# Performance work log

Measured on AMD Instinct MI355X. Metric: run time of the kernel, lower is better.

The kernel has to match this reference:

```python
import jax, jax.numpy as jnp
import numpy as np

N_NODES = 100000
DIM = 64
N_EDGES = 1250000
PRESERVE = 0.1  # preserve_ratio in GCN module


def gcn_conv(x, W, b, row, col, edge_w, num_nodes):
    """PyG GCNConv with normalize=True: symmetric norm with added self-loops.
    x: [N, d], W: [d, d_out], edge (row -> col) with weight edge_w: [E].
    """
    # add self-loops with weight 1
    loop = jnp.arange(num_nodes, dtype=row.dtype)
    r = jnp.concatenate([row, loop])
    c = jnp.concatenate([col, loop])
    w = jnp.concatenate([edge_w, jnp.ones((num_nodes,), dtype=edge_w.dtype)])
    # symmetric degree normalization: deg computed at target (col)
    deg = jax.ops.segment_sum(w, c, num_segments=num_nodes)
    dinv = jnp.where(deg > 0, jax.lax.rsqrt(deg), 0.0)
    norm = dinv[r] * w * dinv[c]  # [E+N]
    xw = x @ W  # [N, d_out] (linear transform before propagation)
    msg = xw[r] * norm[:, None]  # gather + scale
    out = jax.ops.segment_sum(msg, c, num_segments=num_nodes)  # scatter-add at targets
    return out + b


def setup_inputs() -> dict:
    key = jax.random.key(0)
    ks = jax.random.split(key, 8)
    skill_embed = jax.random.normal(ks[0], (N_NODES, DIM), dtype=jnp.float32)
    edge_index = jax.random.randint(ks[1], (2, N_EDGES), 0, N_NODES, dtype=jnp.int64)
    edge_attr = jax.random.uniform(ks[2], (N_EDGES,), dtype=jnp.float32)
    # GCNConv params (W stored as [in, out] here), glorot-ish init
    scale = 1.0 / np.sqrt(DIM)
    W1 = jax.random.uniform(ks[3], (DIM, DIM), minval=-scale, maxval=scale, dtype=jnp.float32)
    b1 = jnp.zeros((DIM,), dtype=jnp.float32)
    W2 = jax.random.uniform(ks[4], (DIM, DIM), minval=-scale, maxval=scale, dtype=jnp.float32)
    b2 = jnp.zeros((DIM,), dtype=jnp.float32)
    return {"skill_embed": skill_embed, "edge_index": edge_index, "edge_attr": edge_attr,
            "W1": W1, "b1": b1, "W2": W2, "b2": b2}


def reference(skill_embed, edge_index, edge_attr, W1, b1, W2, b2):
    row, col = edge_index[0], edge_index[1]
    n = skill_embed.shape[0]
    temp = skill_embed
    out = gcn_conv(skill_embed, W1, b1, row, col, edge_attr, n)
    temp = (1.0 - PRESERVE) * out + PRESERVE * temp
    out = gcn_conv(temp, W2, b2, row, col, edge_attr, n)
    temp = (1.0 - PRESERVE) * out + PRESERVE * temp
    return temp
```

## Files before the change

kernel.cpp:

```cpp
#include <hip/hip_runtime.h>

#define DIM 64
#define PRESERVE 0.1f

typedef unsigned short bf16_t;

__device__ __forceinline__ float readlane_f(float v, int l) {
    return __int_as_float(__builtin_amdgcn_readlane(__float_as_int(v), l));
}
__device__ __forceinline__ float bf2f(bf16_t u) {
    return __uint_as_float(((unsigned)u) << 16);
}
__device__ __forceinline__ bf16_t f2bf(float f) {
    unsigned u = __float_as_uint(f);
    unsigned r = (u + 0x7FFFu + ((u >> 16) & 1u)) >> 16;
    return (bf16_t)r;
}

__global__ void k_init(int* cursor, int n) {
    int i = blockIdx.x * blockDim.x + threadIdx.x;
    if (i < n) cursor[i] = 0;
}

__global__ void k_hist4(const int4* __restrict__ col4, int* cursor,
                        int4* __restrict__ rank4, int nthreads) {
    int t = blockIdx.x * blockDim.x + threadIdx.x;
    if (t >= nthreads) return;
    int4 c = col4[t];
    int4 r;
    r.x = atomicAdd(&cursor[c.x], 1);
    r.y = atomicAdd(&cursor[c.y], 1);
    r.z = atomicAdd(&cursor[c.z], 1);
    r.w = atomicAdd(&cursor[c.w], 1);
    rank4[t] = r;
}

__global__ void k_hist1(const int* __restrict__ col, int* cursor,
                        int* __restrict__ rank, int E) {
    int e = blockIdx.x * blockDim.x + threadIdx.x;
    if (e < E) rank[e] = atomicAdd(&cursor[col[e]], 1);
}

__global__ __launch_bounds__(256) void k_scan1(const int* __restrict__ counts,
                                               int* __restrict__ offsets,
                                               int* __restrict__ blksum, int n) {
    __shared__ int s[256];
    int t = threadIdx.x;
    int idx = blockIdx.x * 256 + t;
    int v = (idx < n) ? counts[idx] : 0;
    s[t] = v;
    __syncthreads();
    for (int off = 1; off < 256; off <<= 1) {
        int x = (t >= off) ? s[t - off] : 0;
        __syncthreads();
        s[t] += x;
        __syncthreads();
    }
    if (idx < n) offsets[idx] = s[t];
    if (t == 255) blksum[blockIdx.x] = s[255];
}

__global__ __launch_bounds__(512) void k_scan2(const int* __restrict__ blksum,
                                               int* __restrict__ blkoff, int nblk) {
    __shared__ int s[512];
    int t = threadIdx.x;
    int v = (t < nblk) ? blksum[t] : 0;
    s[t] = v;
    __syncthreads();
    for (int off = 1; off < 512; off <<= 1) {
        int x = (t >= off) ? s[t - off] : 0;
        __syncthreads();
        s[t] += x;
        __syncthreads();
    }
    if (t < nblk) blkoff[t] = s[t] - v;
}

__global__ __launch_bounds__(256) void k_scan3(const int* __restrict__ counts,
                                               int* __restrict__ offsets,
                                               const int* __restrict__ blkoff,
                                               int n, int E) {
    int t = threadIdx.x;
    int idx = blockIdx.x * 256 + t;
    if (idx < n) offsets[idx] = offsets[idx] - counts[idx] + blkoff[blockIdx.x];
    if (idx == 0) offsets[n] = E;
}

__global__ void k_fill4(const int4* __restrict__ row4, const int4* __restrict__ col4,
                        const float4* __restrict__ w4, const int4* __restrict__ rank4,
                        const int* __restrict__ offsets, int2* __restrict__ sedge,
                        int nthreads) {
    int t = blockIdx.x * blockDim.x + threadIdx.x;
    if (t >= nthreads) return;
    int4 r = row4[t];
    int4 c = col4[t];
    float4 w = w4[t];
    int4 k = rank4[t];
    int2 p;
    p.x = r.x; p.y = __float_as_int(w.x); sedge[offsets[c.x] + k.x] = p;
    p.x = r.y; p.y = __float_as_int(w.y); sedge[offsets[c.y] + k.y] = p;
    p.x = r.z; p.y = __float_as_int(w.z); sedge[offsets[c.z] + k.z] = p;
    p.x = r.w; p.y = __float_as_int(w.w); sedge[offsets[c.w] + k.w] = p;
}

__global__ void k_fill1(const int* __restrict__ row, const int* __restrict__ col,
                        const float* __restrict__ w, const int* __restrict__ rank,
                        const int* __restrict__ offsets, int2* __restrict__ sedge,
                        int E) {
    int e = blockIdx.x * blockDim.x + threadIdx.x;
    if (e >= E) return;
    int2 p;
    p.x = row[e];
    p.y = __float_as_int(w[e]);
    sedge[offsets[col[e]] + rank[e]] = p;
}

__global__ __launch_bounds__(256) void k_deg_seg(const int2* __restrict__ sedge,
                                                 const int* __restrict__ offsets,
                                                 float* __restrict__ dinv, int n) {
    int tid = threadIdx.x;
    int lane = tid & 63;
    int c = blockIdx.x * 4 + (tid >> 6);
    if (c >= n) return;
    int beg = offsets[c];
    int end = offsets[c + 1];
    float s = 0.0f;
    for (int j = beg + lane; j < end; j += 64) s += __int_as_float(sedge[j].y);
    for (int off = 32; off > 0; off >>= 1) s += __shfl_xor(s, off);
    if (lane == 0) {
        float d = 1.0f + s;
        dinv[c] = (d > 0.0f) ? rsqrtf(d) : 0.0f;
    }
}

__global__ __launch_bounds__(256) void k_mm(
        const float* __restrict__ x, const float* __restrict__ W,
        const float* __restrict__ dinv, bf16_t* __restrict__ xs, int n) {
    int tid = threadIdx.x;
    int lane = tid & 63;
    int waveId = blockIdx.x * 4 + (tid >> 6);
    int nWaves = gridDim.x * 4;

    float Wr[DIM];
#pragma unroll
    for (int k = 0; k < DIM; ++k) Wr[k] = W[k * DIM + lane];

    for (int r0 = waveId * 4; r0 < n; r0 += nWaves * 4) {
        if (r0 + 3 < n) {
            float x0 = x[(size_t)(r0 + 0) * DIM + lane];
            float x1 = x[(size_t)(r0 + 1) * DIM + lane];
            float x2 = x[(size_t)(r0 + 2) * DIM + lane];
            float x3 = x[(size_t)(r0 + 3) * DIM + lane];
            float a0 = 0.f, a1 = 0.f, a2 = 0.f, a3 = 0.f;
#pragma unroll
            for (int k = 0; k < DIM; ++k) {
                float w = Wr[k];
                a0 += readlane_f(x0, k) * w;
                a1 += readlane_f(x1, k) * w;
                a2 += readlane_f(x2, k) * w;
                a3 += readlane_f(x3, k) * w;
            }
            xs[(size_t)(r0 + 0) * DIM + lane] = f2bf(a0 * dinv[r0 + 0]);
            xs[(size_t)(r0 + 1) * DIM + lane] = f2bf(a1 * dinv[r0 + 1]);
            xs[(size_t)(r0 + 2) * DIM + lane] = f2bf(a2 * dinv[r0 + 2]);
            xs[(size_t)(r0 + 3) * DIM + lane] = f2bf(a3 * dinv[r0 + 3]);
        } else {
            for (int r = r0; r < n; ++r) {
                float xv = x[(size_t)r * DIM + lane];
                float a = 0.f;
#pragma unroll
                for (int k = 0; k < DIM; ++k) a += readlane_f(xv, k) * Wr[k];
                xs[(size_t)r * DIM + lane] = f2bf(a * dinv[r]);
            }
        }
    }
}

__global__ __launch_bounds__(256) void k_gather(
        const bf16_t* __restrict__ xs, const int* __restrict__ offsets,
        const int2* __restrict__ sedge, const float* __restrict__ dinv,
        const float* __restrict__ b, const float* __restrict__ xprev,
        float* __restrict__ out, int n) {
    int tid = threadIdx.x;
    int lane = tid & 63;
    int c = blockIdx.x * 4 + (tid >> 6);
    if (c >= n) return;
    float di = dinv[c];
    float acc = bf2f(xs[(size_t)c * DIM + lane]);
    int beg = offsets[c];
    int end = offsets[c + 1];
    for (int b0 = beg; b0 < end; b0 += 64) {
        int m = end - b0;
        if (m > 64) m = 64;
        int r_l = 0, w_l = 0;
        if (lane < m) {
            int2 p = sedge[b0 + lane];
            r_l = p.x;
            w_l = p.y;
        }
        int j = 0;
        for (; j + 3 < m; j += 4) {
            int r0 = __builtin_amdgcn_readlane(r_l, j);
            int r1 = __builtin_amdgcn_readlane(r_l, j + 1);
            int r2 = __builtin_amdgcn_readlane(r_l, j + 2);
            int r3 = __builtin_amdgcn_readlane(r_l, j + 3);
            float w0 = readlane_f(__int_as_float(w_l), j);
            float w1 = readlane_f(__int_as_float(w_l), j + 1);
            float w2 = readlane_f(__int_as_float(w_l), j + 2);
            float w3 = readlane_f(__int_as_float(w_l), j + 3);
            float a0 = bf2f(xs[(size_t)r0 * DIM + lane]);
            float a1 = bf2f(xs[(size_t)r1 * DIM + lane]);
            float a2 = bf2f(xs[(size_t)r2 * DIM + lane]);
            float a3 = bf2f(xs[(size_t)r3 * DIM + lane]);
            acc += a0 * w0;
            acc += a1 * w1;
            acc += a2 * w2;
            acc += a3 * w3;
        }
        for (; j < m; ++j) {
            int r0 = __builtin_amdgcn_readlane(r_l, j);
            float w0 = readlane_f(__int_as_float(w_l), j);
            acc += bf2f(xs[(size_t)r0 * DIM + lane]) * w0;
        }
    }
    float v = (1.0f - PRESERVE) * (acc * di + b[lane]) + PRESERVE * xprev[(size_t)c * DIM + lane];
    out[(size_t)c * DIM + lane] = v;
}

extern "C" void kernel_launch(void* const* d_in, const int* in_sizes, int n_in,
                              void* d_out, int out_size, void* d_ws, size_t ws_size,
                              hipStream_t stream) {
    const float* x  = (const float*)d_in[0];
    const int*   ei = (const int*)d_in[1];
    const float* ew = (const float*)d_in[2];
    const float* W1 = (const float*)d_in[3];
    const float* b1 = (const float*)d_in[4];
    const float* W2 = (const float*)d_in[5];
    const float* b2 = (const float*)d_in[6];

    const int N = in_sizes[0] / DIM;
    const int E = in_sizes[2];
    const int* row = ei;
    const int* col = ei + E;

    int2* sedge   = (int2*)d_ws;
    float* dinv   = (float*)(sedge + E);
    float* temp   = dinv + N;
    bf16_t* xs    = (bf16_t*)(temp + (size_t)N * DIM);
    int* rank     = (int*)(xs + (size_t)N * DIM);
    int* cursor   = rank + E;
    int* offsets  = cursor + N;
    int* blksum   = offsets + N + 1;
    int* blkoff   = blksum + 640;

    const int B = 256;
    const int nblkN = (N + B - 1) / B;
    const int nblkG = (N + 3) / 4;
    const int nblkMM = 1024;

    k_init<<<nblkN, B, 0, stream>>>(cursor, N);

    if ((E & 3) == 0) {
        int nt = E / 4;
        k_hist4<<<(nt + B - 1) / B, B, 0, stream>>>((const int4*)col, cursor, (int4*)rank, nt);
    } else {
        k_hist1<<<(E + B - 1) / B, B, 0, stream>>>(col, cursor, rank, E);
    }

    k_scan1<<<nblkN, B, 0, stream>>>(cursor, offsets, blksum, N);
    k_scan2<<<1, 512, 0, stream>>>(blksum, blkoff, nblkN);
    k_scan3<<<nblkN, B, 0, stream>>>(cursor, offsets, blkoff, N, E);

    if ((E & 3) == 0) {
        int nt = E / 4;
        k_fill4<<<(nt + B - 1) / B, B, 0, stream>>>((const int4*)row, (const int4*)col,
                                                    (const float4*)ew, (const int4*)rank,
                                                    offsets, sedge, nt);
    } else {
        k_fill1<<<(E + B - 1) / B, B, 0, stream>>>(row, col, ew, rank, offsets, sedge, E);
    }

    k_deg_seg<<<nblkG, B, 0, stream>>>(sedge, offsets, dinv, N);

    k_mm<<<nblkMM, B, 0, stream>>>(x, W1, dinv, xs, N);
    k_gather<<<nblkG, B, 0, stream>>>(xs, offsets, sedge, dinv, b1, x, temp, N);

    k_mm<<<nblkMM, B, 0, stream>>>(temp, W2, dinv, xs, N);
    k_gather<<<nblkG, B, 0, stream>>>(xs, offsets, sedge, dinv, b2, temp, (float*)d_out, N);
}
```

Measured before the change: 332.9 us.

## Replace per-edge rank array with 8 privatized counter copies for CSR build

The histogram now spreads its atomics over 8 privatized counter arrays chosen by block index, which is meant to cut contention. It no longer stores a per-edge rank. The scan sums the copies and turns each copy into a starting cursor, and the fill pass claims slots with a second round of atomics instead of reading the stored ranks. This drops the rank array traffic but adds atomics to the fill kernel, and the init and scan passes touch 8x more counter memory. Edge order within a segment becomes nondeterministic.

```diff
diff --git a/kernel.cpp b/kernel.cpp
--- a/kernel.cpp
+++ b/kernel.cpp
@@ -2,6 +2,7 @@
 
 #define DIM 64
 #define PRESERVE 0.1f
+#define NCOPY 8
 
 typedef unsigned short bf16_t;
 
@@ -17,37 +18,42 @@
     return (bf16_t)r;
 }
 
-__global__ void k_init(int* cursor, int n) {
+__global__ void k_init(int* cnt8, int n) {
     int i = blockIdx.x * blockDim.x + threadIdx.x;
-    if (i < n) cursor[i] = 0;
-}
-
-__global__ void k_hist4(const int4* __restrict__ col4, int* cursor,
-                        int4* __restrict__ rank4, int nthreads) {
+    if (i < n) cnt8[i] = 0;
+}
+
+__global__ void k_hist4(const int4* __restrict__ col4, int* __restrict__ cnt8,
+                        int nthreads, int N) {
     int t = blockIdx.x * blockDim.x + threadIdx.x;
     if (t >= nthreads) return;
+    int* cur = cnt8 + (size_t)(blockIdx.x & (NCOPY - 1)) * N;
     int4 c = col4[t];
-    int4 r;
-    r.x = atomicAdd(&cursor[c.x], 1);
-    r.y = atomicAdd(&cursor[c.y], 1);
-    r.z = atomicAdd(&cursor[c.z], 1);
-    r.w = atomicAdd(&cursor[c.w], 1);
-    rank4[t] = r;
-}
-
-__global__ void k_hist1(const int* __restrict__ col, int* cursor,
-                        int* __restrict__ rank, int E) {
+    atomicAdd(&cur[c.x], 1);
+    atomicAdd(&cur[c.y], 1);
+    atomicAdd(&cur[c.z], 1);
+    atomicAdd(&cur[c.w], 1);
+}
+
+__global__ void k_hist1(const int* __restrict__ col, int* __restrict__ cnt8,
+                        int E, int N) {
     int e = blockIdx.x * blockDim.x + threadIdx.x;
-    if (e < E) rank[e] = atomicAdd(&cursor[col[e]], 1);
-}
-
-__global__ __launch_bounds__(256) void k_scan1(const int* __restrict__ counts,
+    if (e >= E) return;
+    int* cur = cnt8 + (size_t)(blockIdx.x & (NCOPY - 1)) * N;
+    atomicAdd(&cur[col[e]], 1);
+}
+
+__global__ __launch_bounds__(256) void k_scan1(const int* __restrict__ cnt8,
                                                int* __restrict__ offsets,
                                                int* __restrict__ blksum, int n) {
     __shared__ int s[256];
     int t = threadIdx.x;
     int idx = blockIdx.x * 256 + t;
-    int v = (idx < n) ? counts[idx] : 0;
+    int v = 0;
+    if (idx < n) {
+#pragma unroll
+        for (int x = 0; x < NCOPY; ++x) v += cnt8[(size_t)x * n + idx];
+    }
     s[t] = v;
     __syncthreads();
     for (int off = 1; off < 256; off <<= 1) {
@@ -76,43 +82,57 @@
     if (t < nblk) blkoff[t] = s[t] - v;
 }
 
-__global__ __launch_bounds__(256) void k_scan3(const int* __restrict__ counts,
+__global__ __launch_bounds__(256) void k_scan3(int* __restrict__ cnt8,
                                                int* __restrict__ offsets,
                                                const int* __restrict__ blkoff,
                                                int n, int E) {
-    int t = threadIdx.x;
-    int idx = blockIdx.x * 256 + t;
-    if (idx < n) offsets[idx] = offsets[idx] - counts[idx] + blkoff[blockIdx.x];
+    int idx = blockIdx.x * 256 + threadIdx.x;
     if (idx == 0) offsets[n] = E;
+    if (idx >= n) return;
+    int c[NCOPY];
+    int tot = 0;
+#pragma unroll
+    for (int x = 0; x < NCOPY; ++x) {
+        c[x] = cnt8[(size_t)x * n + idx];
+        tot += c[x];
+    }
+    int off = offsets[idx] - tot + blkoff[blockIdx.x];
+    offsets[idx] = off;
+#pragma unroll
+    for (int x = 0; x < NCOPY; ++x) {
+        cnt8[(size_t)x * n + idx] = off;
+        off += c[x];
+    }
 }
 
 __global__ void k_fill4(const int4* __restrict__ row4, const int4* __restrict__ col4,
-                        const float4* __restrict__ w4, const int4* __restrict__ rank4,
-                        const int* __restrict__ offsets, int2* __restrict__ sedge,
-                        int nthreads) {
+                        const float4* __restrict__ w4, int* __restrict__ cnt8,
+                        int2* __restrict__ sedge, int nthreads, int N) {
     int t = blockIdx.x * blockDim.x + threadIdx.x;
     if (t >= nthreads) return;
+    int* cur = cnt8 + (size_t)(blockIdx.x & (NCOPY - 1)) * N;
     int4 r = row4[t];
     int4 c = col4[t];
     float4 w = w4[t];
-    int4 k = rank4[t];
     int2 p;
-    p.x = r.x; p.y = __float_as_int(w.x); sedge[offsets[c.x] + k.x] = p;
-    p.x = r.y; p.y = __float_as_int(w.y); sedge[offsets[c.y] + k.y] = p;
-    p.x = r.z; p.y = __float_as_int(w.z); sedge[offsets[c.z] + k.z] = p;
-    p.x = r.w; p.y = __float_as_int(w.w); sedge[offsets[c.w] + k.w] = p;
+    int pos;
+    pos = atomicAdd(&cur[c.x], 1); p.x = r.x; p.y = __float_as_int(w.x); sedge[pos] = p;
+    pos = atomicAdd(&cur[c.y], 1); p.x = r.y; p.y = __float_as_int(w.y); sedge[pos] = p;
+    pos = atomicAdd(&cur[c.z], 1); p.x = r.z; p.y = __float_as_int(w.z); sedge[pos] = p;
+    pos = atomicAdd(&cur[c.w], 1); p.x = r.w; p.y = __float_as_int(w.w); sedge[pos] = p;
 }
 
 __global__ void k_fill1(const int* __restrict__ row, const int* __restrict__ col,
-                        const float* __restrict__ w, const int* __restrict__ rank,
-                        const int* __restrict__ offsets, int2* __restrict__ sedge,
-                        int E) {
+                        const float* __restrict__ w, int* __restrict__ cnt8,
+                        int2* __restrict__ sedge, int E, int N) {
     int e = blockIdx.x * blockDim.x + threadIdx.x;
     if (e >= E) return;
+    int* cur = cnt8 + (size_t)(blockIdx.x & (NCOPY - 1)) * N;
+    int pos = atomicAdd(&cur[col[e]], 1);
     int2 p;
     p.x = row[e];
     p.y = __float_as_int(w[e]);
-    sedge[offsets[col[e]] + rank[e]] = p;
+    sedge[pos] = p;
 }
 
 __global__ __launch_bounds__(256) void k_deg_seg(const int2* __restrict__ sedge,
@@ -247,9 +267,8 @@
     float* dinv   = (float*)(sedge + E);
     float* temp   = dinv + N;
     bf16_t* xs    = (bf16_t*)(temp + (size_t)N * DIM);
-    int* rank     = (int*)(xs + (size_t)N * DIM);
-    int* cursor   = rank + E;
-    int* offsets  = cursor + N;
+    int* cnt8     = (int*)(xs + (size_t)N * DIM);
+    int* offsets  = cnt8 + (size_t)NCOPY * N;
     int* blksum   = offsets + N + 1;
     int* blkoff   = blksum + 640;
 
@@ -258,26 +277,25 @@
     const int nblkG = (N + 3) / 4;
     const int nblkMM = 1024;
 
-    k_init<<<nblkN, B, 0, stream>>>(cursor, N);
+    k_init<<<(NCOPY * N + B - 1) / B, B, 0, stream>>>(cnt8, NCOPY * N);
 
     if ((E & 3) == 0) {
         int nt = E / 4;
-        k_hist4<<<(nt + B - 1) / B, B, 0, stream>>>((const int4*)col, cursor, (int4*)rank, nt);
+        k_hist4<<<(nt + B - 1) / B, B, 0, stream>>>((const int4*)col, cnt8, nt, N);
     } else {
-        k_hist1<<<(E + B - 1) / B, B, 0, stream>>>(col, cursor, rank, E);
-    }
-
-    k_scan1<<<nblkN, B, 0, stream>>>(cursor, offsets, blksum, N);
+        k_hist1<<<(E + B - 1) / B, B, 0, stream>>>(col, cnt8, E, N);
+    }
+
+    k_scan1<<<nblkN, B, 0, stream>>>(cnt8, offsets, blksum, N);
     k_scan2<<<1, 512, 0, stream>>>(blksum, blkoff, nblkN);
-    k_scan3<<<nblkN, B, 0, stream>>>(cursor, offsets, blkoff, N, E);
+    k_scan3<<<nblkN, B, 0, stream>>>(cnt8, offsets, blkoff, N, E);
 
     if ((E & 3) == 0) {
         int nt = E / 4;
         k_fill4<<<(nt + B - 1) / B, B, 0, stream>>>((const int4*)row, (const int4*)col,
-                                                    (const float4*)ew, (const int4*)rank,
-                                                    offsets, sedge, nt);
+                                                    (const float4*)ew, cnt8, sedge, nt, N);
     } else {
-        k_fill1<<<(E + B - 1) / B, B, 0, stream>>>(row, col, ew, rank, offsets, sedge, E);
+        k_fill1<<<(E + B - 1) / B, B, 0, stream>>>(row, col, ew, cnt8, sedge, E, N);
     }
 
     k_deg_seg<<<nblkG, B, 0, stream>>>(sedge, offsets, dinv, N);
```

Measured after the change: 403.3 us. +21.1%, slower.

## Replace global-atomic counting sort with two-pass bucketed LDS radix CSR build

Applied to the files above, without the earlier changes.

Replaces the CSR construction, which used per-node global atomic histogramming, a three-kernel scan, a random scatter and a separate degree kernel, with a two-level counting sort. Edges are first bucketed by col>>8 using shared-memory histograms per chunk, then each bucket block builds per-node offsets, degrees and dinv locally in LDS and scatters into the final CSR order. This removes global atomics and highly random global writes, and folds the degree computation into the sort, in exchange for an extra intermediate buffer pass that reuses the temp workspace. It assumes the bucket count is at most 512.

```diff
diff --git a/kernel.cpp b/kernel.cpp
--- a/kernel.cpp
+++ b/kernel.cpp
@@ -2,6 +2,8 @@
 
 #define DIM 64
 #define PRESERVE 0.1f
+#define P_BLK 512
+#define NBMAX 512
 
 typedef unsigned short bf16_t;
 
@@ -17,119 +19,128 @@
     return (bf16_t)r;
 }
 
-__global__ void k_init(int* cursor, int n) {
-    int i = blockIdx.x * blockDim.x + threadIdx.x;
-    if (i < n) cursor[i] = 0;
-}
-
-__global__ void k_hist4(const int4* __restrict__ col4, int* cursor,
-                        int4* __restrict__ rank4, int nthreads) {
-    int t = blockIdx.x * blockDim.x + threadIdx.x;
-    if (t >= nthreads) return;
-    int4 c = col4[t];
-    int4 r;
-    r.x = atomicAdd(&cursor[c.x], 1);
-    r.y = atomicAdd(&cursor[c.y], 1);
-    r.z = atomicAdd(&cursor[c.z], 1);
-    r.w = atomicAdd(&cursor[c.w], 1);
-    rank4[t] = r;
-}
-
-__global__ void k_hist1(const int* __restrict__ col, int* cursor,
-                        int* __restrict__ rank, int E) {
-    int e = blockIdx.x * blockDim.x + threadIdx.x;
-    if (e < E) rank[e] = atomicAdd(&cursor[col[e]], 1);
-}
-
-__global__ __launch_bounds__(256) void k_scan1(const int* __restrict__ counts,
-                                               int* __restrict__ offsets,
-                                               int* __restrict__ blksum, int n) {
-    __shared__ int s[256];
-    int t = threadIdx.x;
-    int idx = blockIdx.x * 256 + t;
-    int v = (idx < n) ? counts[idx] : 0;
+
+__global__ __launch_bounds__(256) void k_bcount(const int* __restrict__ col,
+                                                int* __restrict__ bh,
+                                                int E, int nb, int chunk) {
+    __shared__ int hist[NBMAX];
+    int t = threadIdx.x;
+    for (int i = t; i < nb; i += 256) hist[i] = 0;
+    __syncthreads();
+    int beg = blockIdx.x * chunk;
+    int end = beg + chunk;
+    if (end > E) end = E;
+    for (int i = beg + t; i < end; i += 256) atomicAdd(&hist[col[i] >> 8], 1);
+    __syncthreads();
+    for (int i = t; i < nb; i += 256) bh[(size_t)i * P_BLK + blockIdx.x] = hist[i];
+}
+
+__global__ __launch_bounds__(P_BLK) void k_bscan1(int* __restrict__ bh,
+                                                  int* __restrict__ btot) {
+    __shared__ int s[P_BLK];
+    int t = threadIdx.x;
+    size_t base = (size_t)blockIdx.x * P_BLK;
+    int v = bh[base + t];
     s[t] = v;
     __syncthreads();
+    for (int off = 1; off < P_BLK; off <<= 1) {
+        int x = (t >= off) ? s[t - off] : 0;
+        __syncthreads();
+        s[t] += x;
+        __syncthreads();
+    }
+    bh[base + t] = s[t] - v;
+    if (t == P_BLK - 1) btot[blockIdx.x] = s[P_BLK - 1];
+}
+
+__global__ __launch_bounds__(P_BLK) void k_bscan2(const int* __restrict__ btot,
+                                                  int* __restrict__ bbase,
+                                                  int nb, int E) {
+    __shared__ int s[P_BLK];
+    int t = threadIdx.x;
+    int v = (t < nb) ? btot[t] : 0;
+    s[t] = v;
+    __syncthreads();
+    for (int off = 1; off < P_BLK; off <<= 1) {
+        int x = (t >= off) ? s[t - off] : 0;
+        __syncthreads();
+        s[t] += x;
+        __syncthreads();
+    }
+    if (t < nb) bbase[t] = s[t] - v;
+    if (t == 0) bbase[nb] = E;
+}
+
+__global__ __launch_bounds__(256) void k_bscatter(
+        const int* __restrict__ row, const int* __restrict__ col,
+        const float* __restrict__ ew, const int* __restrict__ bh,
+        const int* __restrict__ bbase, int2* __restrict__ sered,
+        int* __restrict__ colb, int E, int nb, int chunk) {
+    __shared__ int cur[NBMAX];
+    int t = threadIdx.x;
+    for (int i = t; i < nb; i += 256)
+        cur[i] = bbase[i] + bh[(size_t)i * P_BLK + blockIdx.x];
+    __syncthreads();
+    int beg = blockIdx.x * chunk;
+    int end = beg + chunk;
+    if (end > E) end = E;
+    for (int i = beg + t; i < end; i += 256) {
+        int c = col[i];
+        int r = row[i];
+        float w = ew[i];
+        int slot = atomicAdd(&cur[c >> 8], 1);
+        int2 pk;
+        pk.x = r;
+        pk.y = __float_as_int(w);
+        sered[slot] = pk;
+        colb[slot] = c;
+    }
+}
+
+__global__ __launch_bounds__(256) void k_bcsr(
+        const int2* __restrict__ sered, const int* __restrict__ colb,
+        const int* __restrict__ bbase, int2* __restrict__ sedge,
+        int* __restrict__ offsets, float* __restrict__ dinv, int N, int E) {
+    __shared__ int cnt[256];
+    __shared__ float degw[256];
+    __shared__ int sc[256];
+    __shared__ int cur[256];
+    int t = threadIdx.x;
+    int b = blockIdx.x;
+    cnt[t] = 0;
+    degw[t] = 0.0f;
+    __syncthreads();
+    int s0 = bbase[b];
+    int e0 = bbase[b + 1];
+    int nbase = b << 8;
+    for (int i = s0 + t; i < e0; i += 256) {
+        int loc = colb[i] - nbase;
+        atomicAdd(&cnt[loc], 1);
+        atomicAdd(&degw[loc], __int_as_float(sered[i].y));
+    }
+    __syncthreads();
+    int v = cnt[t];
+    sc[t] = v;
+    __syncthreads();
     for (int off = 1; off < 256; off <<= 1) {
-        int x = (t >= off) ? s[t - off] : 0;
-        __syncthreads();
-        s[t] += x;
-        __syncthreads();
-    }
-    if (idx < n) offsets[idx] = s[t];
-    if (t == 255) blksum[blockIdx.x] = s[255];
-}
-
-__global__ __launch_bounds__(512) void k_scan2(const int* __restrict__ blksum,
-                                               int* __restrict__ blkoff, int nblk) {
-    __shared__ int s[512];
-    int t = threadIdx.x;
-    int v = (t < nblk) ? blksum[t] : 0;
-    s[t] = v;
-    __syncthreads();
-    for (int off = 1; off < 512; off <<= 1) {
-        int x = (t >= off) ? s[t - off] : 0;
-        __syncthreads();
-        s[t] += x;
-        __syncthreads();
-    }
-    if (t < nblk) blkoff[t] = s[t] - v;
-}
-
-__global__ __launch_bounds__(256) void k_scan3(const int* __restrict__ counts,
-                                               int* __restrict__ offsets,
-                                               const int* __restrict__ blkoff,
-                                               int n, int E) {
-    int t = threadIdx.x;
-    int idx = blockIdx.x * 256 + t;
-    if (idx < n) offsets[idx] = offsets[idx] - counts[idx] + blkoff[blockIdx.x];
-    if (idx == 0) offsets[n] = E;
-}
-
-__global__ void k_fill4(const int4* __restrict__ row4, const int4* __restrict__ col4,
-                        const float4* __restrict__ w4, const int4* __restrict__ rank4,
-                        const int* __restrict__ offsets, int2* __restrict__ sedge,
-                        int nthreads) {
-    int t = blockIdx.x * blockDim.x + threadIdx.x;
-    if (t >= nthreads) return;
-    int4 r = row4[t];
-    int4 c = col4[t];
-    float4 w = w4[t];
-    int4 k = rank4[t];
-    int2 p;
-    p.x = r.x; p.y = __float_as_int(w.x); sedge[offsets[c.x] + k.x] = p;
-    p.x = r.y; p.y = __float_as_int(w.y); sedge[offsets[c.y] + k.y] = p;
-    p.x = r.z; p.y = __float_as_int(w.z); sedge[offsets[c.z] + k.z] = p;
-    p.x = r.w; p.y = __float_as_int(w.w); sedge[offsets[c.w] + k.w] = p;
-}
-
-__global__ void k_fill1(const int* __restrict__ row, const int* __restrict__ col,
-                        const float* __restrict__ w, const int* __restrict__ rank,
-                        const int* __restrict__ offsets, int2* __restrict__ sedge,
-                        int E) {
-    int e = blockIdx.x * blockDim.x + threadIdx.x;
-    if (e >= E) return;
-    int2 p;
-    p.x = row[e];
-    p.y = __float_as_int(w[e]);
-    sedge[offsets[col[e]] + rank[e]] = p;
-}
-
-__global__ __launch_bounds__(256) void k_deg_seg(const int2* __restrict__ sedge,
-                                                 const int* __restrict__ offsets,
-                                                 float* __restrict__ dinv, int n) {
-    int tid = threadIdx.x;
-    int lane = tid & 63;
-    int c = blockIdx.x * 4 + (tid >> 6);
-    if (c >= n) return;
-    int beg = offsets[c];
-    int end = offsets[c + 1];
-    float s = 0.0f;
-    for (int j = beg + lane; j < end; j += 64) s += __int_as_float(sedge[j].y);
-    for (int off = 32; off > 0; off >>= 1) s += __shfl_xor(s, off);
-    if (lane == 0) {
-        float d = 1.0f + s;
-        dinv[c] = (d > 0.0f) ? rsqrtf(d) : 0.0f;
+        int x = (t >= off) ? sc[t - off] : 0;
+        __syncthreads();
+        sc[t] += x;
+        __syncthreads();
+    }
+    int excl = sc[t] - v;
+    cur[t] = excl;
+    int node = nbase + t;
+    if (node < N) {
+        offsets[node] = s0 + excl;
+        dinv[node] = rsqrtf(1.0f + degw[t]);
+    }
+    if (b == 0 && t == 0) offsets[N] = E;
+    __syncthreads();
+    for (int i = s0 + t; i < e0; i += 256) {
+        int loc = colb[i] - nbase;
+        int slot = atomicAdd(&cur[loc], 1);
+        sedge[s0 + slot] = sered[i];
     }
 }
 
@@ -243,44 +254,30 @@
     const int* row = ei;
     const int* col = ei + E;
 
+    const int nb = (N + 255) >> 8;
+    const int chunk = (E + P_BLK - 1) / P_BLK;
+
     int2* sedge   = (int2*)d_ws;
     float* dinv   = (float*)(sedge + E);
-    float* temp   = dinv + N;
-    bf16_t* xs    = (bf16_t*)(temp + (size_t)N * DIM);
-    int* rank     = (int*)(xs + (size_t)N * DIM);
-    int* cursor   = rank + E;
-    int* offsets  = cursor + N;
-    int* blksum   = offsets + N + 1;
-    int* blkoff   = blksum + 640;
+    bf16_t* xs    = (bf16_t*)(dinv + N);
+    float* temp   = (float*)(xs + (size_t)N * DIM);
+    int2* sered   = (int2*)temp;
+    int* colb     = (int*)(sered + E);
+    int* offsets  = (int*)(temp + (size_t)N * DIM);
+    int* bh       = offsets + N + 1;
+    int* btot     = bh + (size_t)nb * P_BLK;
+    int* bbase    = btot + nb;
 
     const int B = 256;
-    const int nblkN = (N + B - 1) / B;
     const int nblkG = (N + 3) / 4;
     const int nblkMM = 1024;
 
-    k_init<<<nblkN, B, 0, stream>>>(cursor, N);
-
-    if ((E & 3) == 0) {
-        int nt = E / 4;
-        k_hist4<<<(nt + B - 1) / B, B, 0, stream>>>((const int4*)col, cursor, (int4*)rank, nt);
-    } else {
-        k_hist1<<<(E + B - 1) / B, B, 0, stream>>>(col, cursor, rank, E);
-    }
-
-    k_scan1<<<nblkN, B, 0, stream>>>(cursor, offsets, blksum, N);
-    k_scan2<<<1, 512, 0, stream>>>(blksum, blkoff, nblkN);
-    k_scan3<<<nblkN, B, 0, stream>>>(cursor, offsets, blkoff, N, E);
-
-    if ((E & 3) == 0) {
-        int nt = E / 4;
-        k_fill4<<<(nt + B - 1) / B, B, 0, stream>>>((const int4*)row, (const int4*)col,
-                                                    (const float4*)ew, (const int4*)rank,
-                                                    offsets, sedge, nt);
-    } else {
-        k_fill1<<<(E + B - 1) / B, B, 0, stream>>>(row, col, ew, rank, offsets, sedge, E);
-    }
-
-    k_deg_seg<<<nblkG, B, 0, stream>>>(sedge, offsets, dinv, N);
+    k_bcount<<<P_BLK, B, 0, stream>>>(col, bh, E, nb, chunk);
+    k_bscan1<<<nb, P_BLK, 0, stream>>>(bh, btot);
+    k_bscan2<<<1, P_BLK, 0, stream>>>(btot, bbase, nb, E);
+    k_bscatter<<<P_BLK, B, 0, stream>>>(row, col, ew, bh, bbase, sered, colb,
+                                        E, nb, chunk);
+    k_bcsr<<<nb, B, 0, stream>>>(sered, colb, bbase, sedge, offsets, dinv, N, E);
 
     k_mm<<<nblkMM, B, 0, stream>>>(x, W1, dinv, xs, N);
     k_gather<<<nblkG, B, 0, stream>>>(xs, offsets, sedge, dinv, b1, x, temp, N);
```

Result: faster. 297.1 us (-10.8%).
